# Kernel tuning notes

Hardware: AMD Instinct MI355X
Metric: run time of the kernel (lower is better)

The kernel has to match this reference:

```python
import jax, jax.numpy as jnp
import numpy as np

B, N, K, D, L = 8, 1024, 16, 256, 3  # batch, max_node_num, neighbor fan-in, g_hidden_dim, layers


def setup_inputs() -> dict:
    key = jax.random.key(0)
    ks = jax.random.split(key, 14)
    f32 = jnp.float32
    scale = 1.0 / np.sqrt(D).astype(np.float32)
    randn = lambda k, s: jax.random.normal(k, s, dtype=f32)
    lens = jax.random.randint(ks[12], (B,), N // 2, N + 1)
    node_mask = (jnp.arange(N)[None, :] < lens[:, None]).astype(f32)
    return {
        "h0": randn(ks[0], (B, N, D)),
        "c0": randn(ks[1], (B, N, D)),
        "x_in": randn(ks[2], (B, N, D)),
        "x_out": randn(ks[3], (B, N, D)),
        "W_in": randn(ks[4], (4, D, D)) * scale,   # gates stacked: [i, o, f, cell]
        "U_in": randn(ks[5], (4, D, D)) * scale,
        "W_out": randn(ks[6], (4, D, D)) * scale,
        "U_out": randn(ks[7], (4, D, D)) * scale,
        "b": jnp.zeros((4, D), dtype=f32),
        "in_mask": jax.random.randint(ks[8], (B, N, K), 0, 2).astype(f32),
        "out_mask": jax.random.randint(ks[9], (B, N, K), 0, 2).astype(f32),
        "node_mask": node_mask,
        "in_nodes": jax.random.randint(ks[10], (B, N, K), 0, N, dtype=jnp.int32),
        "out_nodes": jax.random.randint(ks[11], (B, N, K), 0, N, dtype=jnp.int32),
        "num_layers": L,
    }


def _gather_agg(h, idx, nb_mask, node_mask):
    # h: [B,N,D], idx: [B,N,K] -> masked sum of neighbor hidden states [B,N,D]
    nb = jax.vmap(lambda hb, ib: hb[ib])(h, idx)           # [B,N,K,D]
    agg = jnp.einsum('bnkd,bnk->bnd', nb, nb_mask)
    return agg * node_mask[..., None]


def reference(h0, c0, x_in, x_out, W_in, U_in, W_out, U_out, b,
              in_mask, out_mask, node_mask, in_nodes, out_nodes, num_layers):
    h, c = h0, c0
    nm = node_mask[..., None]
    for _ in range(num_layers):
        h_in = _gather_agg(h, in_nodes, in_mask, node_mask)
        h_out = _gather_agg(h, out_nodes, out_mask, node_mask)
        # pre-activation for all 4 gates at once: [4,B,N,D]
        pre = (jnp.einsum('bnd,gde->gbne', x_in, W_in)
               + jnp.einsum('bnd,gde->gbne', h_in, U_in)
               + jnp.einsum('bnd,gde->gbne', x_out, W_out)
               + jnp.einsum('bnd,gde->gbne', h_out, U_out)
               + b[:, None, None, :])
        i_g = jax.nn.sigmoid(pre[0])
        o_g = jax.nn.sigmoid(pre[1])
        f_g = jax.nn.sigmoid(pre[2])
        g = jnp.tanh(pre[3])
        c = (f_g * c + i_g * g) * nm
        h = o_g * jnp.tanh(c) * nm
    return h
```

## Files before the change

kernel.cpp:

```cpp
#include <hip/hip_runtime.h>
#include <hip/hip_bf16.h>
#include <cstdint>
#include <cstddef>

typedef __hip_bfloat16 bf16;
typedef _Float16 f16;
typedef __attribute__((ext_vector_type(4))) float f32x4;
typedef __attribute__((ext_vector_type(8))) _Float16 f16x8;

#define BB 8
#define NN 1024
#define KK 16
#define DD 256
#define MM (BB * NN)
#define GW 1024
#define NLAYER 3

__device__ __forceinline__ float ldf(const void* p, size_t i, int isf32) {
  return isf32 ? ((const float*)p)[i] : __bfloat162float(((const bf16*)p)[i]);
}

__device__ __forceinline__ void gload_lds16(const void* g, void* l) {
  __builtin_amdgcn_global_load_lds(
      (const __attribute__((address_space(1))) unsigned int*)g,
      (__attribute__((address_space(3))) unsigned int*)l, 16, 0, 0);
}

__global__ void detect_dtype(const unsigned short* __restrict__ w, int* __restrict__ flag) {
  __shared__ int cnt;
  if (threadIdx.x == 0) cnt = 0;
  __syncthreads();
  int sane = 0;
  for (int i = threadIdx.x; i < 512; i += 256) {
    unsigned short b = w[2 * i];
    int e = (b >> 7) & 0xFF;
    if ((e >= 105 && e <= 130) || (b & 0x7FFF) == 0) sane++;
  }
  atomicAdd(&cnt, sane);
  __syncthreads();
  if (threadIdx.x == 0) flag[0] = (cnt > 256) ? 0 : 1;
}

__global__ void prep(const void* __restrict__ bvec, const void* __restrict__ node_mask,
                     const void* __restrict__ in_mask, const void* __restrict__ out_mask,
                     const void* __restrict__ h0, const void* __restrict__ c0,
                     const void* __restrict__ x_in, const void* __restrict__ x_out,
                     float* __restrict__ biasI, float* __restrict__ nmF,
                     float* __restrict__ inmF, float* __restrict__ outmF,
                     f16* __restrict__ h, f16* __restrict__ c,
                     f16* __restrict__ A, const int* __restrict__ flag) {
  int isf32 = flag[0];
  size_t t = (size_t)blockIdx.x * 256 + threadIdx.x;
  const size_t S0 = 1024;
  const size_t S1 = S0 + MM;
  const size_t S2 = S1 + (size_t)MM * KK;
  const size_t S3 = S2 + (size_t)MM * KK;
  const size_t S4 = S3 + (size_t)MM * DD;
  const size_t S5 = S4 + (size_t)MM * DD;
  if (t < S0) {
    size_t e = t >> 2, g = t & 3;
    biasI[t] = ldf(bvec, g * 256 + e, isf32);
  } else if (t < S1) {
    nmF[t - S0] = ldf(node_mask, t - S0, isf32);
  } else if (t < S2) {
    inmF[t - S1] = ldf(in_mask, t - S1, isf32);
  } else if (t < S3) {
    outmF[t - S2] = ldf(out_mask, t - S2, isf32);
  } else if (t < S4) {
    size_t i = t - S3;
    h[i] = (f16)ldf(h0, i, isf32);
    c[i] = (f16)ldf(c0, i, isf32);
  } else if (t < S5) {
    size_t i = t - S4;
    size_t m = i >> 8, d = i & 255;
    A[m * 1024 + d]       = (f16)ldf(x_in, m * DD + d, isf32);
    A[m * 1024 + 256 + d] = (f16)ldf(x_out, m * DD + d, isf32);
  }
}

__global__ void transpose_w(const void* __restrict__ W_in, const void* __restrict__ W_out,
                            const void* __restrict__ U_in, const void* __restrict__ U_out,
                            f16* __restrict__ BT, const int* __restrict__ flag) {
  int isf32 = flag[0];
  int z = blockIdx.z; int g = z & 3; int which = z >> 2;
  const void* src = (which == 0) ? W_in : (which == 1) ? W_out : (which == 2) ? U_in : U_out;
  int colofs = which * 256;
  size_t gbase = (size_t)g * DD * DD;
  __shared__ float tile[64][65];
  int tx = threadIdx.x & 63, ty = threadIdx.x >> 6;
  int d0 = blockIdx.x * 64, e0 = blockIdx.y * 64;
#pragma unroll
  for (int r = 0; r < 64; r += 4)
    tile[ty + r][tx] = ldf(src, gbase + (size_t)(d0 + ty + r) * DD + e0 + tx, isf32);
  __syncthreads();
#pragma unroll
  for (int r = 0; r < 64; r += 4)
    BT[(size_t)(4 * (e0 + ty + r) + g) * 1024 + colofs + d0 + tx] = (f16)tile[tx][ty + r];
}

__global__ void gather_agg(const f16* __restrict__ h,
                           const int* __restrict__ in_nodes, const int* __restrict__ out_nodes,
                           const float* __restrict__ in_mask, const float* __restrict__ out_mask,
                           const float* __restrict__ node_mask,
                           f16* __restrict__ A) {
  int wave = threadIdx.x >> 6;
  int lane = threadIdx.x & 63;
  int m = blockIdx.x * 4 + wave;
  int l5 = lane & 31, dir = lane >> 5;
  int myidx = 0; float mymask = 0.f;
  if (lane < 16)      { myidx = in_nodes[(size_t)m * KK + lane];
                        mymask = in_mask[(size_t)m * KK + lane]; }
  else if (lane < 32) { myidx = out_nodes[(size_t)m * KK + lane - 16];
                        mymask = out_mask[(size_t)m * KK + lane - 16]; }
  const f16* hb = h + (size_t)(m >> 10) * NN * DD;
  float acc[8] = {};
#pragma unroll
  for (int k = 0; k < KK; k++) {
    int src = dir * 16 + k;
    int idxk = __shfl(myidx, src);
    float wk = __shfl(mymask, src);
    f16x8 v = *(const f16x8*)(hb + (size_t)idxk * DD + l5 * 8);
#pragma unroll
    for (int q = 0; q < 8; q++) acc[q] += wk * (float)v[q];
  }
  float nm = node_mask[m];
  f16x8 o;
#pragma unroll
  for (int q = 0; q < 8; q++) o[q] = (f16)(acc[q] * nm);
  *(f16x8*)(A + (size_t)m * 1024 + 512 + dir * 256 + l5 * 8) = o;
}

#define BM 64
#define BN 128
#define BK 64
#define KTOT 1024
__global__ __launch_bounds__(256, 4)
void gemm_fused(const f16* __restrict__ A, const f16* __restrict__ Bt,
                const float* __restrict__ biasI,
                f16* __restrict__ cbuf, f16* __restrict__ hbuf,
                const float* __restrict__ node_mask,
                void* __restrict__ outp, int last, const int* __restrict__ flag) {
  __shared__ char smem[24576];
  f16*   As   = (f16*)smem;
  f16*   Bs   = (f16*)(smem + 8192);
  float* tile = (float*)smem;

  int t = threadIdx.x;
  int w = t >> 6, lane = t & 63;
  int row16 = lane & 15, kgrp = lane >> 4;
  int mBase = blockIdx.x * BM, nBase = blockIdx.y * BN;

  int aoff[2][4], boff[2][2];
#pragma unroll
  for (int sub = 0; sub < 2; sub++) {
    int ch = ((sub * 4 + kgrp) ^ (row16 & 7)) * 8;
#pragma unroll
    for (int i = 0; i < 4; i++)
      aoff[sub][i] = (row16 + 16 * i) * 64 + ch;
#pragma unroll
    for (int j = 0; j < 2; j++)
      boff[sub][j] = (w * 32 + 16 * j + row16) * 64 + ch;
  }

  int srow = t >> 3;
  int scol = ((t & 7) ^ (srow & 7)) * 8;
  const f16* ga0 = A  + (size_t)(mBase + srow) * 1024 + scol;
  const f16* gb0 = Bt + (size_t)(nBase + srow) * 1024 + scol;

  f32x4 acc[4][2] = {};

  for (int kt = 0; kt < KTOT; kt += BK) {
    const f16* ga = ga0 + kt;
    const f16* gb = gb0 + kt;
#pragma unroll
    for (int q = 0; q < 2; q++)
      gload_lds16(ga + (size_t)(32 * q) * 1024, As + q * 2048 + t * 8);
#pragma unroll
    for (int q = 0; q < 4; q++)
      gload_lds16(gb + (size_t)(32 * q) * 1024, Bs + q * 2048 + t * 8);
    __syncthreads();

#pragma unroll
    for (int sub = 0; sub < 2; sub++) {
      f16x8 af[4], bfr[2];
#pragma unroll
      for (int i = 0; i < 4; i++) af[i] = *(const f16x8*)(As + aoff[sub][i]);
#pragma unroll
      for (int j = 0; j < 2; j++) bfr[j] = *(const f16x8*)(Bs + boff[sub][j]);
#pragma unroll
      for (int i = 0; i < 4; i++)
#pragma unroll
        for (int j = 0; j < 2; j++)
          acc[i][j] = __builtin_amdgcn_mfma_f32_16x16x32_f16(af[i], bfr[j], acc[i][j], 0, 0, 0);
    }
    __syncthreads();
  }

  int isf32 = flag[0];
#pragma unroll
  for (int p = 0; p < 2; p++) {
    __syncthreads();
    if ((w >> 1) == p) {
#pragma unroll
      for (int i = 0; i < 4; i++)
#pragma unroll
        for (int j = 0; j < 2; j++) {
          int cl = (w & 1) * 32 + 16 * j + row16;
#pragma unroll
          for (int r = 0; r < 4; r++) {
            int rr = 16 * i + 4 * kgrp + r;
            int ch = (cl >> 2) ^ (rr & 7);
            tile[rr * 64 + ch * 4 + (cl & 3)] = acc[i][j][r];
          }
        }
    }
    __syncthreads();

    int el = t & 15;
    int nb = nBase + 64 * p;
    int eb = nb >> 2;
    f32x4 bv4 = *(const f32x4*)(biasI + nb + el * 4);
#pragma unroll
    for (int rep = 0; rep < 4; rep++) {
      int ml = rep * 16 + (t >> 4);
      int gm = mBase + ml;
      f32x4 vals = *(const f32x4*)(tile + ml * 64 + ((el ^ (ml & 7))) * 4);
      float nm = node_mask[gm];
      size_t ci = (size_t)gm * DD + eb + el;
      float cold = (float)cbuf[ci];
      float p_i = vals[0] + bv4[0];
      float p_o = vals[1] + bv4[1];
      float p_f = vals[2] + bv4[2];
      float p_g = vals[3] + bv4[3];
      float ig = 1.f / (1.f + expf(-p_i));
      float og = 1.f / (1.f + expf(-p_o));
      float fg = 1.f / (1.f + expf(-p_f));
      float gg = tanhf(p_g);
      float cn = (fg * cold + ig * gg) * nm;
      float hn = og * tanhf(cn) * nm;
      cbuf[ci] = (f16)cn;
      hbuf[ci] = (f16)hn;
      if (last) {
        if (isf32) ((float*)outp)[ci] = hn;
        else       ((bf16*)outp)[ci] = __float2bfloat16(hn);
      }
    }
  }
}

extern "C" void kernel_launch(void* const* d_in, const int* in_sizes, int n_in,
                              void* d_out, int out_size, void* d_ws, size_t ws_size,
                              hipStream_t stream) {
  const void* h0      = d_in[0];
  const void* c0      = d_in[1];
  const void* x_in    = d_in[2];
  const void* x_out   = d_in[3];
  const void* W_in    = d_in[4];
  const void* U_in    = d_in[5];
  const void* W_out   = d_in[6];
  const void* U_out   = d_in[7];
  const void* bvec    = d_in[8];
  const void* in_mask = d_in[9];
  const void* out_mask= d_in[10];
  const void* node_mask = d_in[11];
  const int*  in_nodes  = (const int*)d_in[12];
  const int*  out_nodes = (const int*)d_in[13];

  char* ws = (char*)d_ws;
  int*   flag  = (int*)ws;
  f16*   h_cur = (f16*)(ws + 256);
  f16*   c_cur = h_cur + (size_t)MM * DD;
  f16*   A_buf = c_cur + (size_t)MM * DD;
  f16*   BT    = A_buf + (size_t)MM * 1024;
  float* biasI = (float*)(BT + (size_t)1024 * 1024);
  float* nmF   = biasI + 1024;
  float* inmF  = nmF + MM;
  float* outmF = inmF + (size_t)MM * KK;

  detect_dtype<<<1, 256, 0, stream>>>((const unsigned short*)W_in, flag);

  {
    size_t total = 1024 + MM + 2 * (size_t)MM * KK + 2 * (size_t)MM * DD;
    prep<<<(int)((total + 255) / 256), 256, 0, stream>>>(
        bvec, node_mask, in_mask, out_mask, h0, c0, x_in, x_out,
        biasI, nmF, inmF, outmF, h_cur, c_cur, A_buf, flag);
  }
  transpose_w<<<dim3(4, 4, 16), 256, 0, stream>>>(W_in, W_out, U_in, U_out, BT, flag);

  for (int l = 0; l < NLAYER; l++) {
    gather_agg<<<MM / 4, 256, 0, stream>>>(h_cur, in_nodes, out_nodes,
                                           inmF, outmF, nmF, A_buf);
    gemm_fused<<<dim3(MM / BM, GW / BN), 256, 0, stream>>>(
        A_buf, BT, biasI, c_cur, h_cur, nmF,
        d_out, l == NLAYER - 1, flag);
  }
}
```

Measured before the change: 231.6 us.

## Enlarge GEMM tile to 128x128 and fold dtype detection into each kernel

The fused GEMM+LSTM kernel moves from 64x128 to 128x128 tiles. Each wave now computes a 64x64 sub-tile with a 4x4 MFMA accumulator grid, which raises operand reuse per LDS load and halves the grid size. The standalone dtype-detect kernel is removed, and every kernel instead recomputes the flag per block from W_in, which drops one launch but adds a small read and a sync in every block. The larger accumulator set and 32KB LDS could limit occupancy under the 4-block launch bound.

```diff
diff --git a/kernel.cpp b/kernel.cpp
--- a/kernel.cpp
+++ b/kernel.cpp
@@ -26,30 +26,33 @@
       (__attribute__((address_space(3))) unsigned int*)l, 16, 0, 0);
 }
 
-__global__ void detect_dtype(const unsigned short* __restrict__ w, int* __restrict__ flag) {
-  __shared__ int cnt;
-  if (threadIdx.x == 0) cnt = 0;
+__device__ __forceinline__ int detect_isf32_block(const void* W, int* s_cnt) {
+  if (threadIdx.x == 0) *s_cnt = 0;
   __syncthreads();
+  const unsigned short* w = (const unsigned short*)W;
   int sane = 0;
-  for (int i = threadIdx.x; i < 512; i += 256) {
+  for (int i = threadIdx.x; i < 512; i += blockDim.x) {
     unsigned short b = w[2 * i];
     int e = (b >> 7) & 0xFF;
     if ((e >= 105 && e <= 130) || (b & 0x7FFF) == 0) sane++;
   }
-  atomicAdd(&cnt, sane);
+  atomicAdd(s_cnt, sane);
   __syncthreads();
-  if (threadIdx.x == 0) flag[0] = (cnt > 256) ? 0 : 1;
-}
-
-__global__ void prep(const void* __restrict__ bvec, const void* __restrict__ node_mask,
-                     const void* __restrict__ in_mask, const void* __restrict__ out_mask,
-                     const void* __restrict__ h0, const void* __restrict__ c0,
-                     const void* __restrict__ x_in, const void* __restrict__ x_out,
-                     float* __restrict__ biasI, float* __restrict__ nmF,
-                     float* __restrict__ inmF, float* __restrict__ outmF,
-                     f16* __restrict__ h, f16* __restrict__ c,
-                     f16* __restrict__ A, const int* __restrict__ flag) {
-  int isf32 = flag[0];
+  return (*s_cnt > 256) ? 0 : 1;
+}
+
+struct Params {
+  const void *h0, *c0, *x_in, *x_out, *W_in, *U_in, *W_out, *U_out, *bvec;
+  const void *in_mask, *out_mask, *node_mask;
+  const int *in_nodes, *out_nodes;
+  float *biasI, *nmF, *inmF, *outmF;
+  f16 *h_cur, *c_cur, *A_buf, *BT;
+  void* outp;
+};
+
+__global__ void prep_k(Params p) {
+  __shared__ int s_cnt;
+  int isf32 = detect_isf32_block(p.W_in, &s_cnt);
   size_t t = (size_t)blockIdx.x * 256 + threadIdx.x;
   const size_t S0 = 1024;
   const size_t S1 = S0 + MM;
@@ -59,34 +62,34 @@
   const size_t S5 = S4 + (size_t)MM * DD;
   if (t < S0) {
     size_t e = t >> 2, g = t & 3;
-    biasI[t] = ldf(bvec, g * 256 + e, isf32);
+    p.biasI[t] = ldf(p.bvec, g * 256 + e, isf32);
   } else if (t < S1) {
-    nmF[t - S0] = ldf(node_mask, t - S0, isf32);
+    p.nmF[t - S0] = ldf(p.node_mask, t - S0, isf32);
   } else if (t < S2) {
-    inmF[t - S1] = ldf(in_mask, t - S1, isf32);
+    p.inmF[t - S1] = ldf(p.in_mask, t - S1, isf32);
   } else if (t < S3) {
-    outmF[t - S2] = ldf(out_mask, t - S2, isf32);
+    p.outmF[t - S2] = ldf(p.out_mask, t - S2, isf32);
   } else if (t < S4) {
     size_t i = t - S3;
-    h[i] = (f16)ldf(h0, i, isf32);
-    c[i] = (f16)ldf(c0, i, isf32);
+    p.h_cur[i] = (f16)ldf(p.h0, i, isf32);
+    p.c_cur[i] = (f16)ldf(p.c0, i, isf32);
   } else if (t < S5) {
     size_t i = t - S4;
     size_t m = i >> 8, d = i & 255;
-    A[m * 1024 + d]       = (f16)ldf(x_in, m * DD + d, isf32);
-    A[m * 1024 + 256 + d] = (f16)ldf(x_out, m * DD + d, isf32);
-  }
-}
-
-__global__ void transpose_w(const void* __restrict__ W_in, const void* __restrict__ W_out,
-                            const void* __restrict__ U_in, const void* __restrict__ U_out,
-                            f16* __restrict__ BT, const int* __restrict__ flag) {
-  int isf32 = flag[0];
+    p.A_buf[m * 1024 + d]       = (f16)ldf(p.x_in, m * DD + d, isf32);
+    p.A_buf[m * 1024 + 256 + d] = (f16)ldf(p.x_out, m * DD + d, isf32);
+  }
+}
+
+__global__ void transpose_k(Params p) {
+  __shared__ float tile[64][65];
+  __shared__ int s_cnt;
+  int isf32 = detect_isf32_block(p.W_in, &s_cnt);
   int z = blockIdx.z; int g = z & 3; int which = z >> 2;
-  const void* src = (which == 0) ? W_in : (which == 1) ? W_out : (which == 2) ? U_in : U_out;
+  const void* src = (which == 0) ? p.W_in : (which == 1) ? p.W_out
+                   : (which == 2) ? p.U_in : p.U_out;
   int colofs = which * 256;
   size_t gbase = (size_t)g * DD * DD;
-  __shared__ float tile[64][65];
   int tx = threadIdx.x & 63, ty = threadIdx.x >> 6;
   int d0 = blockIdx.x * 64, e0 = blockIdx.y * 64;
 #pragma unroll
@@ -95,24 +98,20 @@
   __syncthreads();
 #pragma unroll
   for (int r = 0; r < 64; r += 4)
-    BT[(size_t)(4 * (e0 + ty + r) + g) * 1024 + colofs + d0 + tx] = (f16)tile[tx][ty + r];
-}
-
-__global__ void gather_agg(const f16* __restrict__ h,
-                           const int* __restrict__ in_nodes, const int* __restrict__ out_nodes,
-                           const float* __restrict__ in_mask, const float* __restrict__ out_mask,
-                           const float* __restrict__ node_mask,
-                           f16* __restrict__ A) {
+    p.BT[(size_t)(4 * (e0 + ty + r) + g) * 1024 + colofs + d0 + tx] = (f16)tile[tx][ty + r];
+}
+
+__global__ void gather_k(Params p) {
   int wave = threadIdx.x >> 6;
   int lane = threadIdx.x & 63;
   int m = blockIdx.x * 4 + wave;
   int l5 = lane & 31, dir = lane >> 5;
   int myidx = 0; float mymask = 0.f;
-  if (lane < 16)      { myidx = in_nodes[(size_t)m * KK + lane];
-                        mymask = in_mask[(size_t)m * KK + lane]; }
-  else if (lane < 32) { myidx = out_nodes[(size_t)m * KK + lane - 16];
-                        mymask = out_mask[(size_t)m * KK + lane - 16]; }
-  const f16* hb = h + (size_t)(m >> 10) * NN * DD;
+  if (lane < 16)      { myidx = p.in_nodes[(size_t)m * KK + lane];
+                        mymask = p.inmF[(size_t)m * KK + lane]; }
+  else if (lane < 32) { myidx = p.out_nodes[(size_t)m * KK + lane - 16];
+                        mymask = p.outmF[(size_t)m * KK + lane - 16]; }
+  const f16* hb = p.h_cur + (size_t)(m >> 10) * NN * DD;
   float acc[8] = {};
 #pragma unroll
   for (int k = 0; k < KK; k++) {
@@ -123,111 +122,103 @@
 #pragma unroll
     for (int q = 0; q < 8; q++) acc[q] += wk * (float)v[q];
   }
-  float nm = node_mask[m];
+  float nm = p.nmF[m];
   f16x8 o;
 #pragma unroll
   for (int q = 0; q < 8; q++) o[q] = (f16)(acc[q] * nm);
-  *(f16x8*)(A + (size_t)m * 1024 + 512 + dir * 256 + l5 * 8) = o;
-}
-
-#define BM 64
-#define BN 128
-#define BK 64
-#define KTOT 1024
+  *(f16x8*)(p.A_buf + (size_t)m * 1024 + 512 + dir * 256 + l5 * 8) = o;
+}
+
 __global__ __launch_bounds__(256, 4)
-void gemm_fused(const f16* __restrict__ A, const f16* __restrict__ Bt,
-                const float* __restrict__ biasI,
-                f16* __restrict__ cbuf, f16* __restrict__ hbuf,
-                const float* __restrict__ node_mask,
-                void* __restrict__ outp, int last, const int* __restrict__ flag) {
-  __shared__ char smem[24576];
-  f16*   As   = (f16*)smem;
-  f16*   Bs   = (f16*)(smem + 8192);
-  float* tile = (float*)smem;
+void gemm_k(Params p, int last) {
+  __shared__ char smem[32768];
+  __shared__ int s_cnt;
+  f16* As = (f16*)smem;
+  f16* Bs = (f16*)(smem + 16384);
+  float* tileF = (float*)smem;
+
+  int isf32 = detect_isf32_block(p.W_in, &s_cnt);
 
   int t = threadIdx.x;
   int w = t >> 6, lane = t & 63;
   int row16 = lane & 15, kgrp = lane >> 4;
-  int mBase = blockIdx.x * BM, nBase = blockIdx.y * BN;
-
-  int aoff[2][4], boff[2][2];
+  int mBase = blockIdx.x * 128, nBase = blockIdx.y * 128;
+  int wm = (w & 1) * 64, wn = (w >> 1) * 64;
+
+  int aoff[2][4], boff[2][4];
 #pragma unroll
   for (int sub = 0; sub < 2; sub++) {
     int ch = ((sub * 4 + kgrp) ^ (row16 & 7)) * 8;
 #pragma unroll
-    for (int i = 0; i < 4; i++)
-      aoff[sub][i] = (row16 + 16 * i) * 64 + ch;
-#pragma unroll
-    for (int j = 0; j < 2; j++)
-      boff[sub][j] = (w * 32 + 16 * j + row16) * 64 + ch;
+    for (int i = 0; i < 4; i++) {
+      aoff[sub][i] = (wm + row16 + 16 * i) * 64 + ch;
+      boff[sub][i] = (wn + row16 + 16 * i) * 64 + ch;
+    }
   }
 
   int srow = t >> 3;
   int scol = ((t & 7) ^ (srow & 7)) * 8;
-  const f16* ga0 = A  + (size_t)(mBase + srow) * 1024 + scol;
-  const f16* gb0 = Bt + (size_t)(nBase + srow) * 1024 + scol;
-
-  f32x4 acc[4][2] = {};
-
-  for (int kt = 0; kt < KTOT; kt += BK) {
+  const f16* ga0 = p.A_buf + (size_t)(mBase + srow) * 1024 + scol;
+  const f16* gb0 = p.BT + (size_t)(nBase + srow) * 1024 + scol;
+
+  f32x4 acc[4][4] = {};
+
+  for (int kt = 0; kt < 1024; kt += 64) {
     const f16* ga = ga0 + kt;
     const f16* gb = gb0 + kt;
 #pragma unroll
-    for (int q = 0; q < 2; q++)
+    for (int q = 0; q < 4; q++) {
       gload_lds16(ga + (size_t)(32 * q) * 1024, As + q * 2048 + t * 8);
-#pragma unroll
-    for (int q = 0; q < 4; q++)
       gload_lds16(gb + (size_t)(32 * q) * 1024, Bs + q * 2048 + t * 8);
-    __syncthreads();
-
+    }
+    __syncthreads();
 #pragma unroll
     for (int sub = 0; sub < 2; sub++) {
-      f16x8 af[4], bfr[2];
+      f16x8 af[4], bfr[4];
 #pragma unroll
       for (int i = 0; i < 4; i++) af[i] = *(const f16x8*)(As + aoff[sub][i]);
 #pragma unroll
-      for (int j = 0; j < 2; j++) bfr[j] = *(const f16x8*)(Bs + boff[sub][j]);
+      for (int j = 0; j < 4; j++) bfr[j] = *(const f16x8*)(Bs + boff[sub][j]);
 #pragma unroll
       for (int i = 0; i < 4; i++)
 #pragma unroll
-        for (int j = 0; j < 2; j++)
+        for (int j = 0; j < 4; j++)
           acc[i][j] = __builtin_amdgcn_mfma_f32_16x16x32_f16(af[i], bfr[j], acc[i][j], 0, 0, 0);
     }
     __syncthreads();
   }
 
-  int isf32 = flag[0];
-#pragma unroll
-  for (int p = 0; p < 2; p++) {
-    __syncthreads();
-    if ((w >> 1) == p) {
+#pragma unroll
+  for (int pp = 0; pp < 2; pp++) {
+    __syncthreads();
+    if ((w >> 1) == pp) {
 #pragma unroll
       for (int i = 0; i < 4; i++)
 #pragma unroll
-        for (int j = 0; j < 2; j++) {
-          int cl = (w & 1) * 32 + 16 * j + row16;
+        for (int j = 0; j < 4; j++) {
+          int cl = 16 * j + row16;
+          int e = cl >> 2;
 #pragma unroll
           for (int r = 0; r < 4; r++) {
-            int rr = 16 * i + 4 * kgrp + r;
-            int ch = (cl >> 2) ^ (rr & 7);
-            tile[rr * 64 + ch * 4 + (cl & 3)] = acc[i][j][r];
+            int rr = wm + 16 * i + 4 * kgrp + r;
+            tileF[rr * 64 + (e ^ (rr & 7)) * 4 + (cl & 3)] = acc[i][j][r];
           }
         }
     }
     __syncthreads();
 
     int el = t & 15;
-    int nb = nBase + 64 * p;
+    int nb = nBase + 64 * pp;
     int eb = nb >> 2;
-    f32x4 bv4 = *(const f32x4*)(biasI + nb + el * 4);
-#pragma unroll
-    for (int rep = 0; rep < 4; rep++) {
+    f32x4 bv4 = *(const f32x4*)(p.biasI + nb + el * 4);
+#pragma unroll
+    for (int rep = 0; rep < 8; rep++) {
       int ml = rep * 16 + (t >> 4);
       int gm = mBase + ml;
-      f32x4 vals = *(const f32x4*)(tile + ml * 64 + ((el ^ (ml & 7))) * 4);
-      float nm = node_mask[gm];
+      f32x4 vals = *(const f32x4*)(tileF + ml * 64 + ((el ^ (ml & 7))) * 4);
+      float nm = p.nmF[gm];
       size_t ci = (size_t)gm * DD + eb + el;
-      float cold = (float)cbuf[ci];
+      float cold = (float)p.c_cur[ci];
       float p_i = vals[0] + bv4[0];
       float p_o = vals[1] + bv4[1];
       float p_f = vals[2] + bv4[2];
@@ -238,11 +229,11 @@
       float gg = tanhf(p_g);
       float cn = (fg * cold + ig * gg) * nm;
       float hn = og * tanhf(cn) * nm;
-      cbuf[ci] = (f16)cn;
-      hbuf[ci] = (f16)hn;
+      p.c_cur[ci] = (f16)cn;
+      p.h_cur[ci] = (f16)hn;
       if (last) {
-        if (isf32) ((float*)outp)[ci] = hn;
-        else       ((bf16*)outp)[ci] = __float2bfloat16(hn);
+        if (isf32) ((float*)p.outp)[ci] = hn;
+        else       ((bf16*)p.outp)[ci] = __float2bfloat16(hn);
       }
     }
   }
@@ -251,23 +242,7 @@
 extern "C" void kernel_launch(void* const* d_in, const int* in_sizes, int n_in,
                               void* d_out, int out_size, void* d_ws, size_t ws_size,
                               hipStream_t stream) {
-  const void* h0      = d_in[0];
-  const void* c0      = d_in[1];
-  const void* x_in    = d_in[2];
-  const void* x_out   = d_in[3];
-  const void* W_in    = d_in[4];
-  const void* U_in    = d_in[5];
-  const void* W_out   = d_in[6];
-  const void* U_out   = d_in[7];
-  const void* bvec    = d_in[8];
-  const void* in_mask = d_in[9];
-  const void* out_mask= d_in[10];
-  const void* node_mask = d_in[11];
-  const int*  in_nodes  = (const int*)d_in[12];
-  const int*  out_nodes = (const int*)d_in[13];
-
   char* ws = (char*)d_ws;
-  int*   flag  = (int*)ws;
   f16*   h_cur = (f16*)(ws + 256);
   f16*   c_cur = h_cur + (size_t)MM * DD;
   f16*   A_buf = c_cur + (size_t)MM * DD;
@@ -277,21 +252,21 @@
   float* inmF  = nmF + MM;
   float* outmF = inmF + (size_t)MM * KK;
 
-  detect_dtype<<<1, 256, 0, stream>>>((const unsigned short*)W_in, flag);
-
-  {
-    size_t total = 1024 + MM + 2 * (size_t)MM * KK + 2 * (size_t)MM * DD;
-    prep<<<(int)((total + 255) / 256), 256, 0, stream>>>(
-        bvec, node_mask, in_mask, out_mask, h0, c0, x_in, x_out,
-        biasI, nmF, inmF, outmF, h_cur, c_cur, A_buf, flag);
-  }
-  transpose_w<<<dim3(4, 4, 16), 256, 0, stream>>>(W_in, W_out, U_in, U_out, BT, flag);
+  Params p;
+  p.h0 = d_in[0]; p.c0 = d_in[1]; p.x_in = d_in[2]; p.x_out = d_in[3];
+  p.W_in = d_in[4]; p.U_in = d_in[5]; p.W_out = d_in[6]; p.U_out = d_in[7];
+  p.bvec = d_in[8]; p.in_mask = d_in[9]; p.out_mask = d_in[10]; p.node_mask = d_in[11];
+  p.in_nodes = (const int*)d_in[12]; p.out_nodes = (const int*)d_in[13];
+  p.biasI = biasI; p.nmF = nmF; p.inmF = inmF; p.outmF = outmF;
+  p.h_cur = h_cur; p.c_cur = c_cur; p.A_buf = A_buf; p.BT = BT;
+  p.outp = d_out;
+
+  size_t total = 1024 + MM + 2 * (size_t)MM * KK + 2 * (size_t)MM * DD;
+  prep_k<<<(int)((total + 255) / 256), 256, 0, stream>>>(p);
+  transpose_k<<<dim3(4, 4, 16), 256, 0, stream>>>(p);
 
   for (int l = 0; l < NLAYER; l++) {
-    gather_agg<<<MM / 4, 256, 0, stream>>>(h_cur, in_nodes, out_nodes,
-                                           inmF, outmF, nmF, A_buf);
-    gemm_fused<<<dim3(MM / BM, GW / BN), 256, 0, stream>>>(
-        A_buf, BT, biasI, c_cur, h_cur, nmF,
-        d_out, l == NLAYER - 1, flag);
-  }
-}
+    gather_k<<<MM / 4, 256, 0, stream>>>(p);
+    gemm_k<<<dim3(MM / 128, GW / 128), 256, 0, stream>>>(p, l == NLAYER - 1);
+  }
+}
```

New measurement: 300.1 us. 29.6% more time.
